# Performance work log

Measured on AMD Instinct MI355X. Metric: run time of the kernel, lower is better.

## Reference

```python
import jax, jax.numpy as jnp
import numpy as np

B, T_TEXT, T_AUDIO, D = 16, 512, 4096, 256
TEMPERATURE = 10.0


def setup_inputs() -> dict:
    key = jax.random.key(0)
    k1, k2 = jax.random.split(key)
    hidden_state = jax.random.normal(k1, (B, D, T_TEXT), dtype=jnp.float32)
    # monotone token centers in [0, T_AUDIO)
    centers = jnp.sort(
        jax.random.uniform(k2, (B, T_TEXT), dtype=jnp.float32, minval=0.0, maxval=float(T_AUDIO)),
        axis=-1,
    )
    # audio frame timestamps 0..A-1, shared across batch
    audio_timestamps = jnp.broadcast_to(
        jnp.arange(T_AUDIO, dtype=jnp.float32), (B, T_AUDIO)
    )
    return {
        "hidden_state": hidden_state,
        "centers": centers,
        "audio_timestamps": audio_timestamps,
    }


def reference(hidden_state, centers, audio_timestamps):
    # interpolation_weights: squared-distance score, temperature-scaled softmax over tokens
    # centers: [B, T], audio_timestamps: [B, A] -> diffs: [B, A, T]
    diffs = centers[:, None, :] - audio_timestamps[:, :, None]
    logits = (-(TEMPERATURE ** -2)) * jnp.square(diffs)  # [B, A, T]
    weights = jax.nn.softmax(logits, axis=-1)            # softmax over token dim
    # audio_aligned_representation: matmul + sum reduction, fused into one einsum
    # hidden_state: [B, D, T]; contract T with weights, then sum over audio axis A
    out = jnp.einsum("bdt,bat->bd", hidden_state, weights)
    return out
```

## Files before the change

### kernel.cpp

```cpp
#include <hip/hip_runtime.h>

#define B_ 16
#define T_ 512
#define A_ 4096
#define D_ 256
#define NEG_SCALE2 (-0.01f * 1.4426950408889634f)
#define CHUNK 256
#define RADIUS 96.0f
#define PF 16

__global__ __launch_bounds__(256) void k_aligner(const float* __restrict__ centers,
                                                 const float* __restrict__ ats,
                                                 const float* __restrict__ hidden,
                                                 float* __restrict__ out) {
    __shared__ float  sc[T_];
    __shared__ float2 ai[CHUNK];
    __shared__ float  wl[T_];

    const int tid = threadIdx.x;
    const int b  = blockIdx.y;
    const int a0 = blockIdx.x * CHUNK;

    const float c0 = centers[b * T_ + tid];
    const float c1 = centers[b * T_ + tid + 256];
    sc[tid]       = c0;
    sc[tid + 256] = c1;
    wl[tid]       = 0.f;
    wl[tid + 256] = 0.f;
    const float myts = ats[b * A_ + a0 + tid];
    ai[tid] = make_float2(myts, 0.f);
    __syncthreads();

    const float lov = ai[0].x - RADIUS;
    const float hiv = ai[CHUNK - 1].x + RADIUS;
    const int tlo = __syncthreads_count(c0 < lov) + __syncthreads_count(c1 < lov);
    const int thi = T_ - __syncthreads_count(c0 > hiv) - __syncthreads_count(c1 > hiv);

    const int t0 = min(tlo & ~3, T_ - 4 * PF);
    const float* hrow = hidden + (size_t)(b * D_ + tid) * T_;
    const float4* hp4 = (const float4*)(hrow + t0);
    float4 hf[PF];
    #pragma unroll
    for (int i = 0; i < PF; ++i) hf[i] = hp4[i];

    float s0 = 0.f, s1 = 0.f;
    int t = tlo;
    #pragma unroll 4
    for (; t + 1 < thi; t += 2) {
        float d0 = sc[t] - myts;
        float d1 = sc[t + 1] - myts;
        s0 += __builtin_exp2f(NEG_SCALE2 * d0 * d0);
        s1 += __builtin_exp2f(NEG_SCALE2 * d1 * d1);
    }
    if (t < thi) {
        float d = sc[t] - myts;
        s0 += __builtin_exp2f(NEG_SCALE2 * d * d);
    }
    ai[tid].y = 1.0f / fmaxf(s0 + s1, 1e-37f);
    __syncthreads();

    for (int base = tlo; base < thi; base += 64) {
        int tt = base + (tid >> 2);
        if (tt < thi) {
            float c = sc[tt];
            float w0 = 0.f, w1 = 0.f;
            #pragma unroll 4
            for (int k = (tid & 3); k < CHUNK; k += 8) {
                float2 p = ai[k];
                float dp = c - p.x;
                w0 += __builtin_exp2f(NEG_SCALE2 * dp * dp) * p.y;
                float2 q = ai[k + 4];
                float dq = c - q.x;
                w1 += __builtin_exp2f(NEG_SCALE2 * dq * dq) * q.y;
            }
            float w = w0 + w1;
            w += __shfl_xor(w, 1, 64);
            w += __shfl_xor(w, 2, 64);
            if ((tid & 3) == 0) wl[tt] = w;
        }
    }
    __syncthreads();

    const float4* wl4 = (const float4*)wl;
    const int w0i = t0 >> 2;
    float accA = 0.f, accB = 0.f;
    #pragma unroll
    for (int i = 0; i < PF; i += 2) {
        float4 h0 = hf[i],     w0 = wl4[w0i + i];
        float4 h1 = hf[i + 1], w1 = wl4[w0i + i + 1];
        accA += h0.x * w0.x + h0.y * w0.y + h0.z * w0.z + h0.w * w0.w;
        accB += h1.x * w1.x + h1.y * w1.y + h1.z * w1.z + h1.w * w1.w;
    }
    for (int tt = t0 + 4 * PF; tt < thi; ++tt)
        accA += hrow[tt] * wl[tt];

    atomicAdd(&out[b * D_ + tid], accA + accB);
}

extern "C" void kernel_launch(void* const* d_in, const int* in_sizes, int n_in,
                              void* d_out, int out_size, void* d_ws, size_t ws_size,
                              hipStream_t stream) {
    const float* hidden  = (const float*)d_in[0];
    const float* centers = (const float*)d_in[1];
    const float* ats     = (const float*)d_in[2];
    float* out  = (float*)d_out;

    k_aligner<<<dim3(A_ / CHUNK, B_), 256, 0, stream>>>(centers, ats, hidden, out);
}
```

Before: 71.29 us.

## Quadruple threads per block and split each row's work across four lanes

Raises the block size from 256 to 1024 threads and gives each of the normalizer, token-weight and hidden-dot phases four (or sixteen) cooperating lanes, combined with shuffle reductions. Each lane now loads only a quarter of the 64-float hidden window, which cuts register pressure and the serial exp loops per thread. The grid is still only 256 blocks. The trade-offs are extra shuffles, larger per-block barriers, and a correctness risk: the tail loop and the reductions now depend on lane indexing staying consistent.

```diff
diff --git a/kernel.cpp b/kernel.cpp
--- a/kernel.cpp
+++ b/kernel.cpp
@@ -7,12 +7,11 @@
 #define NEG_SCALE2 (-0.01f * 1.4426950408889634f)
 #define CHUNK 256
 #define RADIUS 96.0f
-#define PF 16
 
-__global__ __launch_bounds__(256) void k_aligner(const float* __restrict__ centers,
-                                                 const float* __restrict__ ats,
-                                                 const float* __restrict__ hidden,
-                                                 float* __restrict__ out) {
+__global__ __launch_bounds__(1024) void k_aligner(const float* __restrict__ centers,
+                                                  const float* __restrict__ ats,
+                                                  const float* __restrict__ hidden,
+                                                  float* __restrict__ out) {
     __shared__ float  sc[T_];
     __shared__ float2 ai[CHUNK];
     __shared__ float  wl[T_];
@@ -21,80 +20,90 @@
     const int b  = blockIdx.y;
     const int a0 = blockIdx.x * CHUNK;
 
-    const float c0 = centers[b * T_ + tid];
-    const float c1 = centers[b * T_ + tid + 256];
-    sc[tid]       = c0;
-    sc[tid + 256] = c1;
-    wl[tid]       = 0.f;
-    wl[tid + 256] = 0.f;
-    const float myts = ats[b * A_ + a0 + tid];
-    ai[tid] = make_float2(myts, 0.f);
+    float c = 0.f;
+    if (tid < T_) {
+        c = centers[b * T_ + tid];
+        sc[tid] = c;
+        wl[tid] = 0.f;
+    }
+    if (tid < CHUNK)
+        ai[tid] = make_float2(ats[b * A_ + a0 + tid], 0.f);
     __syncthreads();
 
     const float lov = ai[0].x - RADIUS;
     const float hiv = ai[CHUNK - 1].x + RADIUS;
-    const int tlo = __syncthreads_count(c0 < lov) + __syncthreads_count(c1 < lov);
-    const int thi = T_ - __syncthreads_count(c0 > hiv) - __syncthreads_count(c1 > hiv);
+    const int tlo = __syncthreads_count(tid < T_ && c < lov);
+    const int thi = T_ - __syncthreads_count(tid < T_ && c > hiv);
 
-    const int t0 = min(tlo & ~3, T_ - 4 * PF);
-    const float* hrow = hidden + (size_t)(b * D_ + tid) * T_;
-    const float4* hp4 = (const float4*)(hrow + t0);
-    float4 hf[PF];
-    #pragma unroll
-    for (int i = 0; i < PF; ++i) hf[i] = hp4[i];
+    const int f = tid >> 2;
+    const int q = tid & 3;
 
+    const int t0 = min(tlo & ~3, T_ - 64);
+    const float* hrow = hidden + (size_t)(b * D_ + f) * T_;
+    const float4* hp4 = (const float4*)(hrow + t0) + q * 4;
+    const float4 hf0 = hp4[0], hf1 = hp4[1], hf2 = hp4[2], hf3 = hp4[3];
+
+    const float myts = ai[f].x;
     float s0 = 0.f, s1 = 0.f;
-    int t = tlo;
-    #pragma unroll 4
-    for (; t + 1 < thi; t += 2) {
+    int t = tlo + q;
+    for (; t + 4 < thi; t += 8) {
         float d0 = sc[t] - myts;
-        float d1 = sc[t + 1] - myts;
+        float d1 = sc[t + 4] - myts;
         s0 += __builtin_exp2f(NEG_SCALE2 * d0 * d0);
         s1 += __builtin_exp2f(NEG_SCALE2 * d1 * d1);
     }
     if (t < thi) {
-        float d = sc[t] - myts;
-        s0 += __builtin_exp2f(NEG_SCALE2 * d * d);
+        float d0 = sc[t] - myts;
+        s0 += __builtin_exp2f(NEG_SCALE2 * d0 * d0);
     }
-    ai[tid].y = 1.0f / fmaxf(s0 + s1, 1e-37f);
+    float s = s0 + s1;
+    s += __shfl_xor(s, 1, 64);
+    s += __shfl_xor(s, 2, 64);
+    if (q == 0) ai[f].y = 1.0f / fmaxf(s, 1e-37f);
     __syncthreads();
 
     for (int base = tlo; base < thi; base += 64) {
-        int tt = base + (tid >> 2);
+        int tt = base + (tid >> 4);
         if (tt < thi) {
-            float c = sc[tt];
+            float cc = sc[tt];
             float w0 = 0.f, w1 = 0.f;
-            #pragma unroll 4
-            for (int k = (tid & 3); k < CHUNK; k += 8) {
+            #pragma unroll
+            for (int k = (tid & 15); k < CHUNK; k += 32) {
                 float2 p = ai[k];
-                float dp = c - p.x;
+                float dp = cc - p.x;
                 w0 += __builtin_exp2f(NEG_SCALE2 * dp * dp) * p.y;
-                float2 q = ai[k + 4];
-                float dq = c - q.x;
-                w1 += __builtin_exp2f(NEG_SCALE2 * dq * dq) * q.y;
+                float2 qq = ai[k + 16];
+                float dq = cc - qq.x;
+                w1 += __builtin_exp2f(NEG_SCALE2 * dq * dq) * qq.y;
             }
             float w = w0 + w1;
             w += __shfl_xor(w, 1, 64);
             w += __shfl_xor(w, 2, 64);
-            if ((tid & 3) == 0) wl[tt] = w;
+            w += __shfl_xor(w, 4, 64);
+            w += __shfl_xor(w, 8, 64);
+            if ((tid & 15) == 0) wl[tt] = w;
         }
     }
     __syncthreads();
 
     const float4* wl4 = (const float4*)wl;
-    const int w0i = t0 >> 2;
+    const int wbase = (t0 >> 2) + q * 4;
     float accA = 0.f, accB = 0.f;
-    #pragma unroll
-    for (int i = 0; i < PF; i += 2) {
-        float4 h0 = hf[i],     w0 = wl4[w0i + i];
-        float4 h1 = hf[i + 1], w1 = wl4[w0i + i + 1];
-        accA += h0.x * w0.x + h0.y * w0.y + h0.z * w0.z + h0.w * w0.w;
-        accB += h1.x * w1.x + h1.y * w1.y + h1.z * w1.z + h1.w * w1.w;
+    {
+        float4 w0 = wl4[wbase + 0], w1 = wl4[wbase + 1];
+        float4 w2 = wl4[wbase + 2], w3 = wl4[wbase + 3];
+        accA += hf0.x * w0.x + hf0.y * w0.y + hf0.z * w0.z + hf0.w * w0.w;
+        accB += hf1.x * w1.x + hf1.y * w1.y + hf1.z * w1.z + hf1.w * w1.w;
+        accA += hf2.x * w2.x + hf2.y * w2.y + hf2.z * w2.z + hf2.w * w2.w;
+        accB += hf3.x * w3.x + hf3.y * w3.y + hf3.z * w3.z + hf3.w * w3.w;
     }
-    for (int tt = t0 + 4 * PF; tt < thi; ++tt)
+    for (int tt = t0 + 64 + q; tt < thi; tt += 4)
         accA += hrow[tt] * wl[tt];
 
-    atomicAdd(&out[b * D_ + tid], accA + accB);
+    float acc = accA + accB;
+    acc += __shfl_xor(acc, 1, 64);
+    acc += __shfl_xor(acc, 2, 64);
+    if (q == 0) atomicAdd(&out[b * D_ + f], acc);
 }
 
 extern "C" void kernel_launch(void* const* d_in, const int* in_sizes, int n_in,
@@ -105,5 +114,5 @@
     const float* ats     = (const float*)d_in[2];
     float* out  = (float*)d_out;
 
-    k_aligner<<<dim3(A_ / CHUNK, B_), 256, 0, stream>>>(centers, ats, hidden, out);
+    k_aligner<<<dim3(A_ / CHUNK, B_), 1024, 0, stream>>>(centers, ats, hidden, out);
 }
```

After: 67.99 us. 1.05x faster.
